# Performance work log

Measured on AMD Instinct MI355X. Metric: run time of the kernel, lower is better.

Reference implementation:

```python
import jax, jax.numpy as jnp
import numpy as np

B, N, EMB, HID, CODE, FEAT, L = 8, 96, 768, 384, 192, 768, 2
NEG = 1e30  # mask_logic constant


def _gru(x, h, Wih, Whh, bih, bhh):
    # torch.nn.GRUCell math; gate order r, z, n
    gi = x @ Wih.T + bih
    gh = h @ Whh.T + bhh
    ir, iz, inn = jnp.split(gi, 3, axis=-1)
    hr, hz, hn = jnp.split(gh, 3, axis=-1)
    r = jax.nn.sigmoid(ir + hr)
    z = jax.nn.sigmoid(iz + hz)
    n = jnp.tanh(inn + r * hn)
    return (1.0 - z) * n + z * h


def _node0(Hl, gc, gp):
    # node 0: C = gru_c(x, 0); P = gru_p(0, x); H1 = C + P
    x0 = Hl[:, 0]
    z0 = jnp.zeros_like(x0)
    h0 = _gru(x0, z0, *gc) + _gru(z0, x0, *gp)
    b, n, d = Hl.shape
    return jnp.zeros((b, n, d), Hl.dtype).at[:, 0].set(h0)


def _dag_scan(Hl, s_mask, aux, Wr0, Wr1, gc, gp, get_w):
    # sequential DAG recurrence: node i attends over nodes < i of the CURRENT layer's outputs
    b, n, d = Hl.shape
    buf0 = _node0(Hl, gc, gp)
    pos = jnp.arange(n)

    def step(buf, inp):
        i, q, s_row, aux_row = inp
        valid = pos < i                                  # growing history slice [:i]
        w = get_w(buf, q, aux_row, valid)                # (B,N), zero for j >= i
        s = s_row[:, :, None]
        V = (buf @ Wr0.T) * s + (buf @ Wr1.T) * (1.0 - s)  # speaker-relation values
        M = jnp.einsum('bn,bnd->bd', w, V)
        hn = _gru(q, M, *gc) + _gru(M, q, *gp)           # C + P
        return buf.at[:, i].set(hn), w

    xs = (jnp.arange(1, n),
          jnp.swapaxes(Hl[:, 1:], 0, 1),
          jnp.swapaxes(s_mask[:, 1:], 0, 1),
          jnp.swapaxes(aux[:, 1:], 0, 1))
    buf, ws = jax.lax.scan(step, buf0, xs)
    return buf, jnp.swapaxes(ws, 0, 1)  # H1 (B,N,D), attn rows 1..N-1 (B,N-1,N)


def _mlp(x, W0, b0, W1, b1):
    # out_mlp with mlp_layers=1 (dropout is identity in eval mode)
    return jax.nn.relu(x @ W0.T + b0) @ W1.T + b1


def _forward(features, adj, s_mask, s_mask_onehot,
             enc_fc1_W, enc_fc1_b, enc_gat_w, enc_gat_b, enc_Wr0, enc_Wr1,
             enc_gruc_Wih, enc_gruc_Whh, enc_gruc_bih, enc_gruc_bhh,
             enc_grup_Wih, enc_grup_Whh, enc_grup_bih, enc_grup_bhh,
             enc_mlp_W0, enc_mlp_b0, enc_mlp_W1, enc_mlp_b1,
             dec_fc1_W, dec_fc1_b, dec_Wr0, dec_Wr1,
             dec_gruc_Wih, dec_gruc_Whh, dec_gruc_bih, dec_gruc_bhh,
             dec_grup_Wih, dec_grup_Whh, dec_grup_bih, dec_grup_bhh,
             dec_mlp_W0, dec_mlp_b0, dec_mlp_W1, dec_mlp_b1,
             lengths):
    b, n, _ = features.shape
    I = jnp.broadcast_to(jnp.eye(n, dtype=features.dtype), (b, n, n))
    # ----- encoder -----
    Hs = [jax.nn.relu(features @ enc_fc1_W.T + enc_fc1_b)]
    adjB_list = [jnp.zeros((b, 1, n), features.dtype)]
    for l in range(L):
        gc = (enc_gruc_Wih[l], enc_gruc_Whh[l], enc_gruc_bih[l], enc_gruc_bhh[l])
        gp = (enc_grup_Wih[l], enc_grup_Whh[l], enc_grup_bih[l], enc_grup_bhh[l])
        wq, wk, gb = enc_gat_w[l, :HID], enc_gat_w[l, HID:], enc_gat_b[l]

        def get_w(buf, q, adj_row, valid, wq=wq, wk=wk, gb=gb):
            # GAT_encoder: alpha = Linear([q; K]) masked by adj over history (mask_logic)
            alpha = buf @ wk + (q @ wq)[:, None] + gb
            alpha = alpha - (1.0 - adj_row) * NEG
            alpha = jnp.where(valid[None, :], alpha, -jnp.inf)
            return jax.nn.softmax(alpha, axis=-1)

        H1, ws = _dag_scan(Hs[l], s_mask, adj, enc_Wr0[l], enc_Wr1[l], gc, gp, get_w)
        Hs.append(H1)
        # row 0 of adjB is zeros; rows 1..N-1 are zero-padded attention weights
        adjB_list.append(jnp.concatenate([jnp.zeros((b, 1, n), features.dtype), ws], axis=1))
    fU = _mlp(jnp.concatenate(Hs, axis=-1), enc_mlp_W0, enc_mlp_b0, enc_mlp_W1, enc_mlp_b1)
    # ----- decoder -----
    Hs = [jax.nn.relu(fU @ dec_fc1_W.T + dec_fc1_b)]
    for l in range(L):
        gc = (dec_gruc_Wih[l], dec_gruc_Whh[l], dec_gruc_bih[l], dec_gruc_bhh[l])
        gp = (dec_grup_Wih[l], dec_grup_Whh[l], dec_grup_bih[l], dec_grup_bhh[l])
        b_inv = jnp.linalg.solve(I, I - adjB_list[l + 1])

        def get_w(buf, q, w_row, valid):
            # GNN_decoder: uses b_inv[:, i, :i] directly as gather weights
            return jnp.where(valid[None, :], w_row, 0.0)

        H1, _ = _dag_scan(Hs[l], s_mask, b_inv, dec_Wr0[l], dec_Wr1[l], gc, gp, get_w)
        Hs.append(H1)
    logits = _mlp(jnp.concatenate(Hs, axis=-1), dec_mlp_W0, dec_mlp_b0, dec_mlp_W1, dec_mlp_b1)
    feature_map = jnp.linalg.solve(I, I - adjB_list[2])
    return logits, feature_map


def setup_inputs() -> dict:
    key = jax.random.key(0)
    ks = iter(jax.random.split(key, 48))

    def rn(*shape):
        return jax.random.normal(next(ks), shape, jnp.float32) * 0.05

    return dict(
        features=jax.random.normal(next(ks), (B, N, EMB), jnp.float32),
        adj=jax.random.randint(next(ks), (B, N, N), 0, 2).astype(jnp.float32),
        s_mask=jax.random.randint(next(ks), (B, N, N), 0, 2).astype(jnp.float32),
        s_mask_onehot=jnp.zeros((B, N, N, 2), jnp.float32),
        lengths=jax.random.randint(next(ks), (B,), 1, N),
        enc_fc1_W=rn(HID, EMB), enc_fc1_b=rn(HID),
        enc_gat_w=rn(L, 2 * HID), enc_gat_b=rn(L),
        enc_Wr0=rn(L, HID, HID), enc_Wr1=rn(L, HID, HID),
        enc_gruc_Wih=rn(L, 3 * HID, HID), enc_gruc_Whh=rn(L, 3 * HID, HID),
        enc_gruc_bih=rn(L, 3 * HID), enc_gruc_bhh=rn(L, 3 * HID),
        enc_grup_Wih=rn(L, 3 * HID, HID), enc_grup_Whh=rn(L, 3 * HID, HID),
        enc_grup_bih=rn(L, 3 * HID), enc_grup_bhh=rn(L, 3 * HID),
        enc_mlp_W0=rn(HID, (L + 1) * HID), enc_mlp_b0=rn(HID),
        enc_mlp_W1=rn(CODE, HID), enc_mlp_b1=rn(CODE),
        dec_fc1_W=rn(HID, CODE), dec_fc1_b=rn(HID),
        dec_Wr0=rn(L, HID, HID), dec_Wr1=rn(L, HID, HID),
        dec_gruc_Wih=rn(L, 3 * HID, HID), dec_gruc_Whh=rn(L, 3 * HID, HID),
        dec_gruc_bih=rn(L, 3 * HID), dec_gruc_bhh=rn(L, 3 * HID),
        dec_grup_Wih=rn(L, 3 * HID, HID), dec_grup_Whh=rn(L, 3 * HID, HID),
        dec_grup_bih=rn(L, 3 * HID), dec_grup_bhh=rn(L, 3 * HID),
        dec_mlp_W0=rn(HID, (L + 1) * HID), dec_mlp_b0=rn(HID),
        dec_mlp_W1=rn(FEAT, HID), dec_mlp_b1=rn(FEAT),
    )


def reference(features, adj, s_mask, s_mask_onehot, lengths,
              enc_fc1_W, enc_fc1_b, enc_gat_w, enc_gat_b, enc_Wr0, enc_Wr1,
              enc_gruc_Wih, enc_gruc_Whh, enc_gruc_bih, enc_gruc_bhh,
              enc_grup_Wih, enc_grup_Whh, enc_grup_bih, enc_grup_bhh,
              enc_mlp_W0, enc_mlp_b0, enc_mlp_W1, enc_mlp_b1,
              dec_fc1_W, dec_fc1_b, dec_Wr0, dec_Wr1,
              dec_gruc_Wih, dec_gruc_Whh, dec_gruc_bih, dec_gruc_bhh,
              dec_grup_Wih, dec_grup_Whh, dec_grup_bih, dec_grup_bhh,
              dec_mlp_W0, dec_mlp_b0, dec_mlp_W1, dec_mlp_b1):
    return _forward(features, adj, s_mask, s_mask_onehot,
                    enc_fc1_W, enc_fc1_b, enc_gat_w, enc_gat_b, enc_Wr0, enc_Wr1,
                    enc_gruc_Wih, enc_gruc_Whh, enc_gruc_bih, enc_gruc_bhh,
                    enc_grup_Wih, enc_grup_Whh, enc_grup_bih, enc_grup_bhh,
                    enc_mlp_W0, enc_mlp_b0, enc_mlp_W1, enc_mlp_b1,
                    dec_fc1_W, dec_fc1_b, dec_Wr0, dec_Wr1,
                    dec_gruc_Wih, dec_gruc_Whh, dec_gruc_bih, dec_gruc_bhh,
                    dec_grup_Wih, dec_grup_Whh, dec_grup_bih, dec_grup_bhh,
                    dec_mlp_W0, dec_mlp_b0, dec_mlp_W1, dec_mlp_b1,
                    lengths)
```

## Files before the change

kernel.cpp:

```cpp
#include <hip/hip_runtime.h>
#include <math.h>

#define B_    8
#define N_    96
#define EMB_  768
#define HID_  384
#define GID_  1152
#define CONC_ 1152
#define CODE_ 192
#define FEAT_ 768
#define NSL_  64
#define SD_   6
#define NRW_  42

__device__ __forceinline__ float sigf(float x) { return 1.0f / (1.0f + expf(-x)); }

__device__ __forceinline__ void atstf(float* p, float v) {
  __hip_atomic_store(p, v, __ATOMIC_RELAXED, __HIP_MEMORY_SCOPE_AGENT);
}
__device__ __forceinline__ float atldf(const float* p) {
  return __hip_atomic_load((float*)p, __ATOMIC_RELAXED, __HIP_MEMORY_SCOPE_AGENT);
}
__device__ __forceinline__ float dot4(float4 a, float4 b) {
  return fmaf(a.x, b.x, fmaf(a.y, b.y, fmaf(a.z, b.z, a.w * b.w)));
}

template<int RELU>
__global__ __launch_bounds__(256)
void gemm_bias(const float* __restrict__ A, int lda,
               const float* __restrict__ W,
               const float* __restrict__ bias,
               float* __restrict__ C, int ldc, int K)
{
  __shared__ float As[16][68];
  __shared__ float Bs[16][68];
  const int tid = threadIdx.x;
  const int m0 = blockIdx.y * 64;
  const int n0 = blockIdx.x * 64;
  const int lr = tid >> 2;
  const int lc = (tid & 3) * 4;
  const int ty = tid >> 4, tx = tid & 15;
  float acc[4][4] = {};
  for (int k0 = 0; k0 < K; k0 += 16) {
    float4 a4 = *(const float4*)(A + (size_t)(m0 + lr) * lda + k0 + lc);
    float4 b4 = *(const float4*)(W + (size_t)(n0 + lr) * K + k0 + lc);
    As[lc+0][lr] = a4.x; As[lc+1][lr] = a4.y; As[lc+2][lr] = a4.z; As[lc+3][lr] = a4.w;
    Bs[lc+0][lr] = b4.x; Bs[lc+1][lr] = b4.y; Bs[lc+2][lr] = b4.z; Bs[lc+3][lr] = b4.w;
    __syncthreads();
#pragma unroll
    for (int k = 0; k < 16; ++k) {
      float av[4], bv[4];
#pragma unroll
      for (int i = 0; i < 4; ++i) av[i] = As[k][ty*4+i];
#pragma unroll
      for (int j = 0; j < 4; ++j) bv[j] = Bs[k][tx*4+j];
#pragma unroll
      for (int i = 0; i < 4; ++i)
#pragma unroll
        for (int j = 0; j < 4; ++j) acc[i][j] = fmaf(av[i], bv[j], acc[i][j]);
    }
    __syncthreads();
  }
#pragma unroll
  for (int i = 0; i < 4; ++i) {
    int m = m0 + ty*4 + i;
#pragma unroll
    for (int j = 0; j < 4; ++j) {
      int n = n0 + tx*4 + j;
      float v = acc[i][j] + bias[n];
      if (RELU) v = fmaxf(v, 0.0f);
      C[(size_t)m * ldc + n] = v;
    }
  }
}

__global__ __launch_bounds__(256)
void gemm_bias2(const float* __restrict__ A,
                const float* __restrict__ W0, const float* __restrict__ b0,
                float* __restrict__ C0,
                const float* __restrict__ W1, const float* __restrict__ b1,
                float* __restrict__ C1)
{
  const float* W    = (blockIdx.z == 0) ? W0 : W1;
  const float* bias = (blockIdx.z == 0) ? b0 : b1;
  float*       C    = (blockIdx.z == 0) ? C0 : C1;
  __shared__ float As[16][68];
  __shared__ float Bs[16][68];
  const int tid = threadIdx.x;
  const int m0 = blockIdx.y * 64;
  const int n0 = blockIdx.x * 64;
  const int lr = tid >> 2;
  const int lc = (tid & 3) * 4;
  const int ty = tid >> 4, tx = tid & 15;
  float acc[4][4] = {};
  for (int k0 = 0; k0 < HID_; k0 += 16) {
    float4 a4 = *(const float4*)(A + (size_t)(m0 + lr) * CONC_ + k0 + lc);
    float4 b4 = *(const float4*)(W + (size_t)(n0 + lr) * HID_ + k0 + lc);
    As[lc+0][lr] = a4.x; As[lc+1][lr] = a4.y; As[lc+2][lr] = a4.z; As[lc+3][lr] = a4.w;
    Bs[lc+0][lr] = b4.x; Bs[lc+1][lr] = b4.y; Bs[lc+2][lr] = b4.z; Bs[lc+3][lr] = b4.w;
    __syncthreads();
#pragma unroll
    for (int k = 0; k < 16; ++k) {
      float av[4], bv[4];
#pragma unroll
      for (int i = 0; i < 4; ++i) av[i] = As[k][ty*4+i];
#pragma unroll
      for (int j = 0; j < 4; ++j) bv[j] = Bs[k][tx*4+j];
#pragma unroll
      for (int i = 0; i < 4; ++i)
#pragma unroll
        for (int j = 0; j < 4; ++j) acc[i][j] = fmaf(av[i], bv[j], acc[i][j]);
    }
    __syncthreads();
  }
#pragma unroll
  for (int i = 0; i < 4; ++i) {
    int m = m0 + ty*4 + i;
#pragma unroll
    for (int j = 0; j < 4; ++j) {
      int n = n0 + tx*4 + j;
      C[(size_t)m * GID_ + n] = acc[i][j] + bias[n];
    }
  }
}

__global__ __launch_bounds__(256)
void prod_kernel(const float* __restrict__ Ac, const float* __restrict__ Ap,
                 const float* __restrict__ W0, const float* __restrict__ W1,
                 float* __restrict__ G)
{
  const float* A = (blockIdx.z < 2) ? Ac : Ap;
  const float* W = (blockIdx.z & 1) ? W1 : W0;
  float* C = G + (size_t)blockIdx.z * GID_ * HID_;
  __shared__ float As[16][68];
  __shared__ float Bs[16][68];
  const int tid = threadIdx.x;
  const int m0 = blockIdx.y * 64;
  const int n0 = blockIdx.x * 64;
  const int lr = tid >> 2;
  const int lc = (tid & 3) * 4;
  const int lr2 = tid & 63, kq = tid >> 6;
  const int ty = tid >> 4, tx = tid & 15;
  float acc[4][4] = {};
  for (int k0 = 0; k0 < HID_; k0 += 16) {
    float4 a4 = *(const float4*)(A + (size_t)(m0 + lr) * HID_ + k0 + lc);
    As[lc+0][lr] = a4.x; As[lc+1][lr] = a4.y; As[lc+2][lr] = a4.z; As[lc+3][lr] = a4.w;
#pragma unroll
    for (int u = 0; u < 4; ++u) {
      int kl = kq * 4 + u;
      Bs[kl][lr2] = W[(size_t)(k0 + kl) * HID_ + n0 + lr2];
    }
    __syncthreads();
#pragma unroll
    for (int k = 0; k < 16; ++k) {
      float av[4], bv[4];
#pragma unroll
      for (int i = 0; i < 4; ++i) av[i] = As[k][ty*4+i];
#pragma unroll
      for (int j = 0; j < 4; ++j) bv[j] = Bs[k][tx*4+j];
#pragma unroll
      for (int i = 0; i < 4; ++i)
#pragma unroll
        for (int j = 0; j < 4; ++j) acc[i][j] = fmaf(av[i], bv[j], acc[i][j]);
    }
    __syncthreads();
  }
#pragma unroll
  for (int i = 0; i < 4; ++i)
#pragma unroll
    for (int j = 0; j < 4; ++j)
      C[(size_t)(m0 + ty*4 + i) * HID_ + n0 + tx*4 + j] = acc[i][j];
}

struct ScanP {
  const float* Hl;
  float*       bufC;
  float*       hnX;
  const float* G;
  const float* GIc;
  const float* GHp;
  const float* bhhc;
  const float* bihp;
  const float* Wr0;
  const float* Wr1;
  const float* wk;
  const float* mask;
  const float* smask;
  float*       adjB;
};

template<int ENC>
__global__ __launch_bounds__(256, 2)
void scan_kernel(ScanP p)
{
  const int tid  = threadIdx.x;
  const int b    = blockIdx.x >> 6;
  const int sl   = blockIdx.x & 63;
  const int j0   = sl * SD_;
  const int team = tid >> 4, lane = tid & 15;

  __shared__ __align__(16) float stage[HID_];
  __shared__ float ws0[N_], ws1[N_], s_sm[N_];
  __shared__ float alpha[N_];
  __shared__ float dots[48];
  __shared__ float red4a[4], red4b[4];
  __shared__ float sh_aknew;
  __shared__ float PA[NRW_ * 97];
  __shared__ float PB[NRW_ * 97];

  for (int k = tid; k < NRW_ * 97; k += 256) { PA[k] = 0.f; PB[k] = 0.f; }

  float4 wAr[3][6], wBr[3][6];
#pragma unroll
  for (int u = 0; u < 3; ++u) {
    const int r = team + 16 * u;
    const float *Aptr, *Bptr;
    if (r < 36) {
      const int g = r / 6, jl = r % 6;
      const size_t off = (size_t)((g % 3) * HID_ + j0 + jl) * HID_;
      const float* base = p.G + (g < 3 ? 0 : 2) * (size_t)GID_ * HID_;
      Aptr = base + off;
      Bptr = base + (size_t)GID_ * HID_ + off;
    } else if (r < 42) {
      const int jl = r - 36;
      Aptr = p.Wr0 + (size_t)(j0 + jl) * HID_;
      Bptr = p.Wr1 + (size_t)(j0 + jl) * HID_;
    } else if (r == 42 && ENC) {
      Aptr = p.wk; Bptr = p.wk;
    } else {
      Aptr = p.Wr0; Bptr = p.Wr1;
    }
#pragma unroll
    for (int m = 0; m < 6; ++m) {
      wAr[u][m] = ((const float4*)Aptr)[lane + 16*m];
      wBr[u][m] = ((const float4*)Bptr)[lane + 16*m];
    }
  }
  float bh0=0, bh1=0, bh2=0, bi0=0, bi1=0, bi2=0;
  if (tid < SD_) {
    int j = j0 + tid;
    bh0 = p.bhhc[j]; bh1 = p.bhhc[HID_ + j]; bh2 = p.bhhc[2*HID_ + j];
    bi0 = p.bihp[j]; bi1 = p.bihp[HID_ + j]; bi2 = p.bihp[2*HID_ + j];
  }

#define BULK_STAGE(SRC)                                                      \
  do {                                                                       \
    if (tid < NSL_) {                                                        \
      const float* f_ = (SRC) + tid * SD_;                                   \
      while (__float_as_uint(atldf(f_)) == 0xFFFFFFFFu) {}                   \
    }                                                                        \
    __syncthreads();                                                         \
    {                                                                        \
      float v0 = atldf((SRC) + tid);                                         \
      while (__float_as_uint(v0) == 0xFFFFFFFFu) v0 = atldf((SRC) + tid);    \
      stage[tid] = v0;                                                       \
      if (tid < HID_ - 256) {                                                \
        float v1 = atldf((SRC) + 256 + tid);                                 \
        while (__float_as_uint(v1) == 0xFFFFFFFFu)                           \
          v1 = atldf((SRC) + 256 + tid);                                     \
        stage[256 + tid] = v1;                                               \
      }                                                                      \
    }                                                                        \
    __syncthreads();                                                         \
  } while (0)

  if (tid < SD_) {
    int j = j0 + tid;
    const float* gi = p.GIc + (size_t)(b * N_) * GID_;
    const float* gh = p.GHp + (size_t)(b * N_) * GID_;
    float rc = sigf(gi[j] + bh0);
    float zc = sigf(gi[HID_ + j] + bh1);
    float nc = tanhf(gi[2*HID_ + j] + rc * bh2);
    float outc = (1.0f - zc) * nc;
    float rp = sigf(bi0 + gh[j]);
    float zp = sigf(bi1 + gh[HID_ + j]);
    float np = tanhf(bi2 + rp * gh[2*HID_ + j]);
    float x0 = p.Hl[(size_t)(b * N_) * CONC_ + j];
    float h0 = outc + (1.0f - zp) * np + zp * x0;
    p.bufC[(size_t)(b * N_) * CONC_ + j] = h0;
    atstf(&p.hnX[(size_t)(b * N_) * HID_ + j], h0);
  }
  __syncthreads();

  for (int i = 1; i < N_; ++i) {
    float pf_gi0=0, pf_gi1=0, pf_gi2=0, pf_gh0=0, pf_gh1=0, pf_gh2=0, pf_q=0;
    if (tid < SD_) {
      int j = j0 + tid;
      const float* gi = p.GIc + ((size_t)b * N_ + i) * GID_;
      const float* gh = p.GHp + ((size_t)b * N_ + i) * GID_;
      pf_gi0 = gi[j]; pf_gi1 = gi[HID_ + j]; pf_gi2 = gi[2*HID_ + j];
      pf_gh0 = gh[j]; pf_gh1 = gh[HID_ + j]; pf_gh2 = gh[2*HID_ + j];
      pf_q   = p.Hl[((size_t)b * N_ + i) * CONC_ + j];
    }
    float pf_mrow = 0.0f;
    if (tid < N_) {
      pf_mrow = p.mask[((size_t)b * N_ + i) * N_ + tid];
      s_sm[tid] = p.smask[((size_t)b * N_ + i) * N_ + tid];
    }

    const float* srcH = p.hnX + (size_t)(b * N_ + (i - 1)) * HID_;
    BULK_STAGE(srcH);
    const float4* st4 = (const float4*)stage;
    float4 hreg[6];
#pragma unroll
    for (int m = 0; m < 6; ++m) hreg[m] = st4[lane + 16*m];

#pragma unroll
    for (int u = 0; u < 3; ++u) {
      const int r = team + 16 * u;
      float a = 0.f, bv = 0.f;
#pragma unroll
      for (int m = 0; m < 6; ++m) {
        a  += dot4(wAr[u][m], hreg[m]);
        bv += dot4(wBr[u][m], hreg[m]);
      }
#pragma unroll
      for (int mm = 8; mm; mm >>= 1) {
        a  += __shfl_xor(a, mm);
        bv += __shfl_xor(bv, mm);
      }
      if (lane == 0) {
        if (r < NRW_) { PA[r * 97 + (i - 1)] = a; PB[r * 97 + (i - 1)] = bv; }
        else if (ENC && r == 42) sh_aknew = a;
      }
    }
    __syncthreads();

    if (ENC) {
      if (tid == 0) alpha[i - 1] = sh_aknew;
      float av = -3.0e38f;
      if (tid < i) {
        float ak = (tid == i - 1) ? sh_aknew : alpha[tid];
        av = ak - (1.0f - pf_mrow) * 1e30f;
      }
      float v = av;
#pragma unroll
      for (int m = 32; m; m >>= 1) v = fmaxf(v, __shfl_xor(v, m));
      if ((tid & 63) == 0) red4a[tid >> 6] = v;
      __syncthreads();
      float mx = fmaxf(fmaxf(red4a[0], red4a[1]), fmaxf(red4a[2], red4a[3]));
      float e = (tid < i) ? expf(av - mx) : 0.0f;
      v = e;
#pragma unroll
      for (int m = 32; m; m >>= 1) v += __shfl_xor(v, m);
      if ((tid & 63) == 0) red4b[tid >> 6] = v;
      __syncthreads();
      float ssum = red4b[0] + red4b[1] + red4b[2] + red4b[3];
      if (tid < N_) {
        float w = (tid < i) ? e / ssum : 0.0f;
        float sv = s_sm[tid];
        ws0[tid] = w * sv;
        ws1[tid] = w - w * sv;
        if (sl == 0) p.adjB[((size_t)b * N_ + i) * N_ + tid] = w;
      }
      __syncthreads();
    } else {
      if (tid < N_) {
        float w = (tid < i) ? -pf_mrow : 0.0f;
        float sv = s_sm[tid];
        ws0[tid] = w * sv;
        ws1[tid] = w - w * sv;
      }
      __syncthreads();
    }

    {
      float wsr0[6], wsr1[6];
#pragma unroll
      for (int k = 0; k < 6; ++k) {
        wsr0[k] = ws0[lane + 16*k];
        wsr1[k] = ws1[lane + 16*k];
      }
#pragma unroll
      for (int u = 0; u < 3; ++u) {
        const int r = team + 16 * u;
        if (r < NRW_) {
          float acc = 0.f;
#pragma unroll
          for (int k = 0; k < 6; ++k) {
            int n = lane + 16*k;
            acc = fmaf(wsr0[k], PA[r * 97 + n], fmaf(wsr1[k], PB[r * 97 + n], acc));
          }
#pragma unroll
          for (int mm = 8; mm; mm >>= 1) acc += __shfl_xor(acc, mm);
          if (lane == 0) dots[r] = acc;
        }
      }
    }
    __syncthreads();

    if (tid < SD_) {
      int j = j0 + tid;
      float Mj = dots[36 + tid];
      float rc = sigf(pf_gi0 + dots[tid] + bh0);
      float zc = sigf(pf_gi1 + dots[6 + tid] + bh1);
      float nc = tanhf(pf_gi2 + rc * (dots[12 + tid] + bh2));
      float outc = (1.0f - zc) * nc + zc * Mj;
      float rp = sigf(dots[18 + tid] + bi0 + pf_gh0);
      float zp = sigf(dots[24 + tid] + bi1 + pf_gh1);
      float np = tanhf(dots[30 + tid] + bi2 + rp * pf_gh2);
      float hv = outc + (1.0f - zp) * np + zp * pf_q;
      p.bufC[((size_t)b * N_ + i) * CONC_ + j] = hv;
      atstf(&p.hnX[((size_t)b * N_ + i) * HID_ + j], hv);
    }
    __syncthreads();
  }
#undef BULK_STAGE
}

__global__ __launch_bounds__(256)
void fmap_kernel(const float* __restrict__ adjB2, float* __restrict__ out)
{
  int idx = blockIdx.x * 256 + threadIdx.x;
  if (idx < B_ * N_ * N_) {
    int j = idx % N_;
    int i = (idx / N_) % N_;
    float a = (i == 0) ? 0.0f : adjB2[idx];
    out[idx] = ((i == j) ? 1.0f : 0.0f) - a;
  }
}

extern "C" void kernel_launch(void* const* d_in, const int* in_sizes, int n_in,
                              void* d_out, int out_size, void* d_ws, size_t ws_size,
                              hipStream_t stream)
{
  (void)in_sizes; (void)n_in; (void)out_size; (void)ws_size;
  const float* features     = (const float*)d_in[0];
  const float* adj          = (const float*)d_in[1];
  const float* s_mask       = (const float*)d_in[2];
  const float* enc_fc1_W    = (const float*)d_in[5];
  const float* enc_fc1_b    = (const float*)d_in[6];
  const float* enc_gat_w    = (const float*)d_in[7];
  const float* enc_Wr0      = (const float*)d_in[9];
  const float* enc_Wr1      = (const float*)d_in[10];
  const float* enc_gruc_Wih = (const float*)d_in[11];
  const float* enc_gruc_Whh = (const float*)d_in[12];
  const float* enc_gruc_bih = (const float*)d_in[13];
  const float* enc_gruc_bhh = (const float*)d_in[14];
  const float* enc_grup_Wih = (const float*)d_in[15];
  const float* enc_grup_Whh = (const float*)d_in[16];
  const float* enc_grup_bih = (const float*)d_in[17];
  const float* enc_grup_bhh = (const float*)d_in[18];
  const float* enc_mlp_W0   = (const float*)d_in[19];
  const float* enc_mlp_b0   = (const float*)d_in[20];
  const float* enc_mlp_W1   = (const float*)d_in[21];
  const float* enc_mlp_b1   = (const float*)d_in[22];
  const float* dec_fc1_W    = (const float*)d_in[23];
  const float* dec_fc1_b    = (const float*)d_in[24];
  const float* dec_Wr0      = (const float*)d_in[25];
  const float* dec_Wr1      = (const float*)d_in[26];
  const float* dec_gruc_Wih = (const float*)d_in[27];
  const float* dec_gruc_Whh = (const float*)d_in[28];
  const float* dec_gruc_bih = (const float*)d_in[29];
  const float* dec_gruc_bhh = (const float*)d_in[30];
  const float* dec_grup_Wih = (const float*)d_in[31];
  const float* dec_grup_Whh = (const float*)d_in[32];
  const float* dec_grup_bih = (const float*)d_in[33];
  const float* dec_grup_bhh = (const float*)d_in[34];
  const float* dec_mlp_W0   = (const float*)d_in[35];
  const float* dec_mlp_b0   = (const float*)d_in[36];
  const float* dec_mlp_W1   = (const float*)d_in[37];
  const float* dec_mlp_b1   = (const float*)d_in[38];

  float* ws = (float*)d_ws;
  size_t o = 0;
  float* Hse   = ws + o; o += (size_t)B_ * N_ * CONC_;
  float* Hsd   = ws + o; o += (size_t)B_ * N_ * CONC_;
  float* GIc   = ws + o; o += (size_t)B_ * N_ * GID_;
  float* GHp   = ws + o; o += (size_t)B_ * N_ * GID_;
  float* adjB1 = ws + o; o += (size_t)B_ * N_ * N_;
  float* adjB2 = ws + o; o += (size_t)B_ * N_ * N_;
  float* fU    = ws + o; o += (size_t)B_ * N_ * CODE_;
  float* Tmp   = ws + o; o += (size_t)B_ * N_ * HID_;
  float* hnX4  = ws + o; o += (size_t)4 * B_ * N_ * HID_;
  float* Gbuf  = ws + o; o += (size_t)4 * GID_ * HID_;
  const size_t hn_elems = (size_t)B_ * N_ * HID_;

  const dim3 blk(256);
  float* logits = (float*)d_out;
  float* fmap   = (float*)d_out + (size_t)B_ * N_ * FEAT_;

  hipMemsetAsync(hnX4, 0xFF, 4 * hn_elems * sizeof(float), stream);

  gemm_bias<1><<<dim3(6, 12), blk, 0, stream>>>(features, EMB_, enc_fc1_W, enc_fc1_b,
                                                Hse, CONC_, EMB_);
  for (int l = 0; l < 2; ++l) {
    const float* Hl = Hse + l * HID_;
    gemm_bias2<<<dim3(18, 12, 2), blk, 0, stream>>>(Hl,
        enc_gruc_Wih + (size_t)l * GID_ * HID_, enc_gruc_bih + l * GID_, GIc,
        enc_grup_Whh + (size_t)l * GID_ * HID_, enc_grup_bhh + l * GID_, GHp);
    prod_kernel<<<dim3(6, 18, 4), blk, 0, stream>>>(
        enc_gruc_Whh + (size_t)l * GID_ * HID_, enc_grup_Wih + (size_t)l * GID_ * HID_,
        enc_Wr0 + (size_t)l * HID_ * HID_, enc_Wr1 + (size_t)l * HID_ * HID_, Gbuf);
    ScanP p;
    p.Hl = Hl; p.bufC = Hse + (l + 1) * HID_;
    p.hnX = hnX4 + (size_t)l * hn_elems; p.G = Gbuf;
    p.GIc = GIc; p.GHp = GHp;
    p.bhhc = enc_gruc_bhh + l * GID_;
    p.bihp = enc_grup_bih + l * GID_;
    p.Wr0 = enc_Wr0 + (size_t)l * HID_ * HID_;
    p.Wr1 = enc_Wr1 + (size_t)l * HID_ * HID_;
    p.wk = enc_gat_w + l * 2 * HID_ + HID_;
    p.mask = adj; p.smask = s_mask;
    p.adjB = (l == 0) ? adjB1 : adjB2;
    scan_kernel<1><<<dim3(512), blk, 0, stream>>>(p);
  }
  gemm_bias<1><<<dim3(6, 12), blk, 0, stream>>>(Hse, CONC_, enc_mlp_W0, enc_mlp_b0,
                                                Tmp, HID_, CONC_);
  gemm_bias<0><<<dim3(3, 12), blk, 0, stream>>>(Tmp, HID_, enc_mlp_W1, enc_mlp_b1,
                                                fU, CODE_, HID_);
  gemm_bias<1><<<dim3(6, 12), blk, 0, stream>>>(fU, CODE_, dec_fc1_W, dec_fc1_b,
                                                Hsd, CONC_, CODE_);
  for (int l = 0; l < 2; ++l) {
    const float* Hl = Hsd + l * HID_;
    gemm_bias2<<<dim3(18, 12, 2), blk, 0, stream>>>(Hl,
        dec_gruc_Wih + (size_t)l * GID_ * HID_, dec_gruc_bih + l * GID_, GIc,
        dec_grup_Whh + (size_t)l * GID_ * HID_, dec_grup_bhh + l * GID_, GHp);
    prod_kernel<<<dim3(6, 18, 4), blk, 0, stream>>>(
        dec_gruc_Whh + (size_t)l * GID_ * HID_, dec_grup_Wih + (size_t)l * GID_ * HID_,
        dec_Wr0 + (size_t)l * HID_ * HID_, dec_Wr1 + (size_t)l * HID_ * HID_, Gbuf);
    ScanP p;
    p.Hl = Hl; p.bufC = Hsd + (l + 1) * HID_;
    p.hnX = hnX4 + (size_t)(2 + l) * hn_elems; p.G = Gbuf;
    p.GIc = GIc; p.GHp = GHp;
    p.bhhc = dec_gruc_bhh + l * GID_;
    p.bihp = dec_grup_bih + l * GID_;
    p.Wr0 = dec_Wr0 + (size_t)l * HID_ * HID_;
    p.Wr1 = dec_Wr1 + (size_t)l * HID_ * HID_;
    p.wk = nullptr;
    p.mask = (l == 0) ? adjB1 : adjB2;
    p.smask = s_mask;
    p.adjB = nullptr;
    scan_kernel<0><<<dim3(512), blk, 0, stream>>>(p);
  }
  gemm_bias<1><<<dim3(6, 12), blk, 0, stream>>>(Hsd, CONC_, dec_mlp_W0, dec_mlp_b0,
                                                Tmp, HID_, CONC_);
  gemm_bias<0><<<dim3(12, 12), blk, 0, stream>>>(Tmp, HID_, dec_mlp_W1, dec_mlp_b1,
                                                 logits, FEAT_, HID_);
  fmap_kernel<<<dim3((B_ * N_ * N_ + 255) / 256), blk, 0, stream>>>(adjB2, fmap);
}
```

Baseline: 1.900 ms.

## Fuse both DAG layers into one wavefront-pipelined scan kernel

Merges the two per-layer sequential scan kernels into a single kernel that computes layer-1 node t-1 in the same iteration as layer-0 node t. Layer-1 input projections are computed inline from the staged layer-0 output instead of by a separate GEMM. The shared history buffers are stored as bf16 so two layers' worth fit in LDS. This removes a kernel launch and a full serial pass per encoder/decoder. The cost is that weights are now read from global memory every step rather than held in registers, and bf16 history reduces precision.

```diff
diff --git a/kernel.cpp b/kernel.cpp
--- a/kernel.cpp
+++ b/kernel.cpp
@@ -12,6 +12,7 @@
 #define NSL_  64
 #define SD_   6
 #define NRW_  42
+#define HP_   98
 
 __device__ __forceinline__ float sigf(float x) { return 1.0f / (1.0f + expf(-x)); }
 
@@ -23,6 +24,14 @@
 }
 __device__ __forceinline__ float dot4(float4 a, float4 b) {
   return fmaf(a.x, b.x, fmaf(a.y, b.y, fmaf(a.z, b.z, a.w * b.w)));
+}
+__device__ __forceinline__ unsigned short f2bf(float f) {
+  unsigned u = __float_as_uint(f);
+  u += 0x7fffu + ((u >> 16) & 1u);
+  return (unsigned short)(u >> 16);
+}
+__device__ __forceinline__ float bfu(unsigned short s) {
+  return __uint_as_float(((unsigned)s) << 16);
 }
 
 template<int RELU>
@@ -172,26 +181,115 @@
       C[(size_t)(m0 + ty*4 + i) * HID_ + n0 + tx*4 + j] = acc[i][j];
 }
 
-struct ScanP {
-  const float* Hl;
-  float*       bufC;
-  float*       hnX;
-  const float* G;
-  const float* GIc;
-  const float* GHp;
-  const float* bhhc;
-  const float* bihp;
-  const float* Wr0;
-  const float* Wr1;
-  const float* wk;
-  const float* mask;
-  const float* smask;
-  float*       adjB;
+struct Scan2P {
+  const float* Hl0; float* bufC0; float* bufC1;
+  float* hnX0; float* hnX1;
+  const float* G0; const float* G1;
+  const float* GIc; const float* GHp;
+  const float* bhhc0; const float* bihp0;
+  const float* Wr00; const float* Wr10; const float* wk0;
+  const float* Wr01; const float* Wr11; const float* wk1;
+  const float* Wihc1; const float* bihc1;
+  const float* Whhp1; const float* bhhp1;
+  const float* bhhc1; const float* bihp1;
+  const float* mask0; const float* mask1; const float* smask;
+  float* adjB0; float* adjB1o;
 };
+
+__device__ __forceinline__ void bulk_stage(const float* src, float* stg, int tid)
+{
+  if (tid < NSL_) {
+    const float* f_ = src + tid * SD_;
+    while (__float_as_uint(atldf(f_)) == 0xFFFFFFFFu) {}
+  }
+  __syncthreads();
+  {
+    float v0 = atldf(src + tid);
+    while (__float_as_uint(v0) == 0xFFFFFFFFu) v0 = atldf(src + tid);
+    stg[tid] = v0;
+    if (tid < HID_ - 256) {
+      float v1 = atldf(src + 256 + tid);
+      while (__float_as_uint(v1) == 0xFFFFFFFFu) v1 = atldf(src + 256 + tid);
+      stg[256 + tid] = v1;
+    }
+  }
+  __syncthreads();
+}
+
+template<int ENC>
+__device__ __forceinline__ void make_w(
+    int i, int tid, float pf_m, float* alpha, const float* s_sm,
+    float* ws0, float* ws1, float* red4a, float* red4b,
+    const float* shak, float* adjRow)
+{
+  if (ENC) {
+    float ak_new = *shak;
+    if (tid == 0) alpha[i - 1] = ak_new;
+    float av = -3.0e38f;
+    if (tid < i) {
+      float ak = (tid == i - 1) ? ak_new : alpha[tid];
+      av = ak - (1.0f - pf_m) * 1e30f;
+    }
+    float v = av;
+#pragma unroll
+    for (int m = 32; m; m >>= 1) v = fmaxf(v, __shfl_xor(v, m));
+    if ((tid & 63) == 0) red4a[tid >> 6] = v;
+    __syncthreads();
+    float mx = fmaxf(fmaxf(red4a[0], red4a[1]), fmaxf(red4a[2], red4a[3]));
+    float e = (tid < i) ? expf(av - mx) : 0.0f;
+    v = e;
+#pragma unroll
+    for (int m = 32; m; m >>= 1) v += __shfl_xor(v, m);
+    if ((tid & 63) == 0) red4b[tid >> 6] = v;
+    __syncthreads();
+    float ssum = red4b[0] + red4b[1] + red4b[2] + red4b[3];
+    if (tid < N_) {
+      float w = (tid < i) ? e / ssum : 0.0f;
+      float sv = s_sm[tid];
+      ws0[tid] = w * sv;
+      ws1[tid] = w - w * sv;
+      if (adjRow) adjRow[tid] = w;
+    }
+    __syncthreads();
+  } else {
+    if (tid < N_) {
+      float w = (tid < i) ? -pf_m : 0.0f;
+      float sv = s_sm[tid];
+      ws0[tid] = w * sv;
+      ws1[tid] = w - w * sv;
+    }
+    __syncthreads();
+  }
+}
+
+__device__ __forceinline__ void hist_dots(
+    const unsigned short* PA, const unsigned short* PB,
+    const float* ws0, const float* ws1, float* dots, int team, int lane)
+{
+  float wsr0[6], wsr1[6];
+#pragma unroll
+  for (int k = 0; k < 6; ++k) { wsr0[k] = ws0[lane + 16*k]; wsr1[k] = ws1[lane + 16*k]; }
+#pragma unroll
+  for (int u = 0; u < 3; ++u) {
+    const int r = team + 16 * u;
+    if (r < NRW_) {
+      float acc = 0.f;
+#pragma unroll
+      for (int k = 0; k < 6; ++k) {
+        int n = lane + 16*k;
+        acc = fmaf(wsr0[k], bfu(PA[r * HP_ + n]),
+              fmaf(wsr1[k], bfu(PB[r * HP_ + n]), acc));
+      }
+#pragma unroll
+      for (int mm = 8; mm; mm >>= 1) acc += __shfl_xor(acc, mm);
+      if (lane == 0) dots[r] = acc;
+    }
+  }
+}
 
 template<int ENC>
 __global__ __launch_bounds__(256, 2)
-void scan_kernel(ScanP p)
+void scan2_kernel(Scan2P p)
 {
   const int tid  = threadIdx.x;
   const int b    = blockIdx.x >> 6;
@@ -199,213 +297,232 @@
   const int j0   = sl * SD_;
   const int team = tid >> 4, lane = tid & 15;
 
-  __shared__ __align__(16) float stage[HID_];
+  __shared__ __align__(16) float stage0[HID_];
+  __shared__ __align__(16) float stage1[HID_];
+  __shared__ unsigned short PA0[NRW_*HP_], PB0[NRW_*HP_];
+  __shared__ unsigned short PA1[NRW_*HP_], PB1[NRW_*HP_];
   __shared__ float ws0[N_], ws1[N_], s_sm[N_];
-  __shared__ float alpha[N_];
+  __shared__ float alpha0[N_], alpha1[N_];
   __shared__ float dots[48];
+  __shared__ float gdI[18], gdH[18];
   __shared__ float red4a[4], red4b[4];
-  __shared__ float sh_aknew;
-  __shared__ float PA[NRW_ * 97];
-  __shared__ float PB[NRW_ * 97];
-
-  for (int k = tid; k < NRW_ * 97; k += 256) { PA[k] = 0.f; PB[k] = 0.f; }
-
-  float4 wAr[3][6], wBr[3][6];
+  __shared__ float sh_ak;
+
+  for (int k = tid; k < NRW_*HP_; k += 256) { PA0[k]=0; PB0[k]=0; PA1[k]=0; PB1[k]=0; }
+
+  const float4 *pA0[3], *pB0[3], *pA1[3], *pB1[3];
 #pragma unroll
   for (int u = 0; u < 3; ++u) {
     const int r = team + 16 * u;
-    const float *Aptr, *Bptr;
+    const float *A0,*B0,*A1,*B1;
     if (r < 36) {
       const int g = r / 6, jl = r % 6;
       const size_t off = (size_t)((g % 3) * HID_ + j0 + jl) * HID_;
-      const float* base = p.G + (g < 3 ? 0 : 2) * (size_t)GID_ * HID_;
-      Aptr = base + off;
-      Bptr = base + (size_t)GID_ * HID_ + off;
+      const float* b0 = p.G0 + (g < 3 ? 0 : 2) * (size_t)GID_ * HID_;
+      const float* b1 = p.G1 + (g < 3 ? 0 : 2) * (size_t)GID_ * HID_;
+      A0 = b0 + off; B0 = b0 + (size_t)GID_ * HID_ + off;
+      A1 = b1 + off; B1 = b1 + (size_t)GID_ * HID_ + off;
     } else if (r < 42) {
       const int jl = r - 36;
-      Aptr = p.Wr0 + (size_t)(j0 + jl) * HID_;
-      Bptr = p.Wr1 + (size_t)(j0 + jl) * HID_;
+      A0 = p.Wr00 + (size_t)(j0 + jl) * HID_; B0 = p.Wr10 + (size_t)(j0 + jl) * HID_;
+      A1 = p.Wr01 + (size_t)(j0 + jl) * HID_; B1 = p.Wr11 + (size_t)(j0 + jl) * HID_;
     } else if (r == 42 && ENC) {
-      Aptr = p.wk; Bptr = p.wk;
+      A0 = p.wk0; B0 = p.wk0; A1 = p.wk1; B1 = p.wk1;
     } else {
-      Aptr = p.Wr0; Bptr = p.Wr1;
-    }
-#pragma unroll
-    for (int m = 0; m < 6; ++m) {
-      wAr[u][m] = ((const float4*)Aptr)[lane + 16*m];
-      wBr[u][m] = ((const float4*)Bptr)[lane + 16*m];
-    }
-  }
-  float bh0=0, bh1=0, bh2=0, bi0=0, bi1=0, bi2=0;
+      A0 = p.Wr00; B0 = p.Wr10; A1 = p.Wr01; B1 = p.Wr11;
+    }
+    pA0[u]=(const float4*)A0; pB0[u]=(const float4*)B0;
+    pA1[u]=(const float4*)A1; pB1[u]=(const float4*)B1;
+  }
+  const float4 *pGI[2], *pGH[2]; float bGI[2], bGH[2];
+#pragma unroll
+  for (int u = 0; u < 2; ++u) {
+    const int r2 = team + 16 * u;
+    if (r2 < 18) {
+      const int g = r2 / 6, jl = r2 % 6;
+      const size_t row = (size_t)(g * HID_ + j0 + jl);
+      pGI[u] = (const float4*)(p.Wihc1 + row * HID_);
+      pGH[u] = (const float4*)(p.Whhp1 + row * HID_);
+      bGI[u] = p.bihc1[row]; bGH[u] = p.bhhp1[row];
+    } else {
+      pGI[u] = (const float4*)p.Wihc1; pGH[u] = (const float4*)p.Whhp1;
+      bGI[u] = 0.f; bGH[u] = 0.f;
+    }
+  }
+  float c0h0=0,c0h1=0,c0h2=0,c0i0=0,c0i1=0,c0i2=0;
+  float c1h0=0,c1h1=0,c1h2=0,c1i0=0,c1i1=0,c1i2=0;
   if (tid < SD_) {
     int j = j0 + tid;
-    bh0 = p.bhhc[j]; bh1 = p.bhhc[HID_ + j]; bh2 = p.bhhc[2*HID_ + j];
-    bi0 = p.bihp[j]; bi1 = p.bihp[HID_ + j]; bi2 = p.bihp[2*HID_ + j];
-  }
-
-#define BULK_STAGE(SRC)                                                      \
-  do {                                                                       \
-    if (tid < NSL_) {                                                        \
-      const float* f_ = (SRC) + tid * SD_;                                   \
-      while (__float_as_uint(atldf(f_)) == 0xFFFFFFFFu) {}                   \
-    }                                                                        \
-    __syncthreads();                                                         \
-    {                                                                        \
-      float v0 = atldf((SRC) + tid);                                         \
-      while (__float_as_uint(v0) == 0xFFFFFFFFu) v0 = atldf((SRC) + tid);    \
-      stage[tid] = v0;                                                       \
-      if (tid < HID_ - 256) {                                                \
-        float v1 = atldf((SRC) + 256 + tid);                                 \
-        while (__float_as_uint(v1) == 0xFFFFFFFFu)                           \
-          v1 = atldf((SRC) + 256 + tid);                                     \
-        stage[256 + tid] = v1;                                               \
-      }                                                                      \
-    }                                                                        \
-    __syncthreads();                                                         \
-  } while (0)
+    c0h0=p.bhhc0[j]; c0h1=p.bhhc0[HID_+j]; c0h2=p.bhhc0[2*HID_+j];
+    c0i0=p.bihp0[j]; c0i1=p.bihp0[HID_+j]; c0i2=p.bihp0[2*HID_+j];
+    c1h0=p.bhhc1[j]; c1h1=p.bhhc1[HID_+j]; c1h2=p.bhhc1[2*HID_+j];
+    c1i0=p.bihp1[j]; c1i1=p.bihp1[HID_+j]; c1i2=p.bihp1[2*HID_+j];
+  }
 
   if (tid < SD_) {
     int j = j0 + tid;
     const float* gi = p.GIc + (size_t)(b * N_) * GID_;
     const float* gh = p.GHp + (size_t)(b * N_) * GID_;
-    float rc = sigf(gi[j] + bh0);
-    float zc = sigf(gi[HID_ + j] + bh1);
-    float nc = tanhf(gi[2*HID_ + j] + rc * bh2);
+    float rc = sigf(gi[j] + c0h0);
+    float zc = sigf(gi[HID_ + j] + c0h1);
+    float nc = tanhf(gi[2*HID_ + j] + rc * c0h2);
     float outc = (1.0f - zc) * nc;
-    float rp = sigf(bi0 + gh[j]);
-    float zp = sigf(bi1 + gh[HID_ + j]);
-    float np = tanhf(bi2 + rp * gh[2*HID_ + j]);
-    float x0 = p.Hl[(size_t)(b * N_) * CONC_ + j];
+    float rp = sigf(c0i0 + gh[j]);
+    float zp = sigf(c0i1 + gh[HID_ + j]);
+    float np = tanhf(c0i2 + rp * gh[2*HID_ + j]);
+    float x0 = p.Hl0[(size_t)(b * N_) * CONC_ + j];
     float h0 = outc + (1.0f - zp) * np + zp * x0;
-    p.bufC[(size_t)(b * N_) * CONC_ + j] = h0;
-    atstf(&p.hnX[(size_t)(b * N_) * HID_ + j], h0);
+    p.bufC0[(size_t)(b * N_) * CONC_ + j] = h0;
+    atstf(&p.hnX0[(size_t)(b * N_) * HID_ + j], h0);
   }
   __syncthreads();
 
-  for (int i = 1; i < N_; ++i) {
-    float pf_gi0=0, pf_gi1=0, pf_gi2=0, pf_gh0=0, pf_gh1=0, pf_gh2=0, pf_q=0;
-    if (tid < SD_) {
-      int j = j0 + tid;
-      const float* gi = p.GIc + ((size_t)b * N_ + i) * GID_;
-      const float* gh = p.GHp + ((size_t)b * N_ + i) * GID_;
-      pf_gi0 = gi[j]; pf_gi1 = gi[HID_ + j]; pf_gi2 = gi[2*HID_ + j];
-      pf_gh0 = gh[j]; pf_gh1 = gh[HID_ + j]; pf_gh2 = gh[2*HID_ + j];
-      pf_q   = p.Hl[((size_t)b * N_ + i) * CONC_ + j];
-    }
-    float pf_mrow = 0.0f;
-    if (tid < N_) {
-      pf_mrow = p.mask[((size_t)b * N_ + i) * N_ + tid];
-      s_sm[tid] = p.smask[((size_t)b * N_ + i) * N_ + tid];
-    }
-
-    const float* srcH = p.hnX + (size_t)(b * N_ + (i - 1)) * HID_;
-    BULK_STAGE(srcH);
-    const float4* st4 = (const float4*)stage;
-    float4 hreg[6];
-#pragma unroll
-    for (int m = 0; m < 6; ++m) hreg[m] = st4[lane + 16*m];
-
-#pragma unroll
-    for (int u = 0; u < 3; ++u) {
-      const int r = team + 16 * u;
-      float a = 0.f, bv = 0.f;
-#pragma unroll
-      for (int m = 0; m < 6; ++m) {
-        a  += dot4(wAr[u][m], hreg[m]);
-        bv += dot4(wBr[u][m], hreg[m]);
-      }
-#pragma unroll
-      for (int mm = 8; mm; mm >>= 1) {
-        a  += __shfl_xor(a, mm);
-        bv += __shfl_xor(bv, mm);
-      }
-      if (lane == 0) {
-        if (r < NRW_) { PA[r * 97 + (i - 1)] = a; PB[r * 97 + (i - 1)] = bv; }
-        else if (ENC && r == 42) sh_aknew = a;
-      }
-    }
-    __syncthreads();
-
-    if (ENC) {
-      if (tid == 0) alpha[i - 1] = sh_aknew;
-      float av = -3.0e38f;
-      if (tid < i) {
-        float ak = (tid == i - 1) ? sh_aknew : alpha[tid];
-        av = ak - (1.0f - pf_mrow) * 1e30f;
-      }
-      float v = av;
-#pragma unroll
-      for (int m = 32; m; m >>= 1) v = fmaxf(v, __shfl_xor(v, m));
-      if ((tid & 63) == 0) red4a[tid >> 6] = v;
+  for (int t = 1; t <= N_; ++t) {
+    const bool doA = (t < N_);
+    float a_gi0=0,a_gi1=0,a_gi2=0,a_gh0=0,a_gh1=0,a_gh2=0,a_q=0,a_m=0;
+    if (doA) {
+      if (tid < SD_) {
+        int j = j0 + tid;
+        const float* gi = p.GIc + ((size_t)b * N_ + t) * GID_;
+        const float* gh = p.GHp + ((size_t)b * N_ + t) * GID_;
+        a_gi0 = gi[j]; a_gi1 = gi[HID_ + j]; a_gi2 = gi[2*HID_ + j];
+        a_gh0 = gh[j]; a_gh1 = gh[HID_ + j]; a_gh2 = gh[2*HID_ + j];
+        a_q   = p.Hl0[((size_t)b * N_ + t) * CONC_ + j];
+      }
+      if (tid < N_) {
+        a_m = p.mask0[((size_t)b * N_ + t) * N_ + tid];
+        s_sm[tid] = p.smask[((size_t)b * N_ + t) * N_ + tid];
+      }
+    }
+    bulk_stage(p.hnX0 + (size_t)(b * N_ + t - 1) * HID_, stage0, tid);
+    if (doA) {
+      const float4* st = (const float4*)stage0;
+      float4 hr[6];
+#pragma unroll
+      for (int m = 0; m < 6; ++m) hr[m] = st[lane + 16*m];
+#pragma unroll
+      for (int u = 0; u < 3; ++u) {
+        const int r = team + 16 * u;
+        float a = 0.f, bv = 0.f;
+#pragma unroll
+        for (int m = 0; m < 6; ++m) {
+          a  += dot4(pA0[u][lane + 16*m], hr[m]);
+          bv += dot4(pB0[u][lane + 16*m], hr[m]);
+        }
+#pragma unroll
+        for (int mm = 8; mm; mm >>= 1) { a += __shfl_xor(a, mm); bv += __shfl_xor(bv, mm); }
+        if (lane == 0) {
+          if (r < NRW_) { PA0[r*HP_ + (t-1)] = f2bf(a); PB0[r*HP_ + (t-1)] = f2bf(bv); }
+          else if (ENC && r == 42) sh_ak = a;
+        }
+      }
       __syncthreads();
-      float mx = fmaxf(fmaxf(red4a[0], red4a[1]), fmaxf(red4a[2], red4a[3]));
-      float e = (tid < i) ? expf(av - mx) : 0.0f;
-      v = e;
-#pragma unroll
-      for (int m = 32; m; m >>= 1) v += __shfl_xor(v, m);
-      if ((tid & 63) == 0) red4b[tid >> 6] = v;
+      float* adjRow = (ENC && sl == 0) ? (p.adjB0 + ((size_t)b * N_ + t) * N_) : nullptr;
+      make_w<ENC>(t, tid, a_m, alpha0, s_sm, ws0, ws1, red4a, red4b, &sh_ak, adjRow);
+      hist_dots(PA0, PB0, ws0, ws1, dots, team, lane);
       __syncthreads();
-      float ssum = red4b[0] + red4b[1] + red4b[2] + red4b[3];
-      if (tid < N_) {
-        float w = (tid < i) ? e / ssum : 0.0f;
-        float sv = s_sm[tid];
-        ws0[tid] = w * sv;
-        ws1[tid] = w - w * sv;
-        if (sl == 0) p.adjB[((size_t)b * N_ + i) * N_ + tid] = w;
+      if (tid < SD_) {
+        int j = j0 + tid;
+        float Mj = dots[36 + tid];
+        float rc = sigf(a_gi0 + dots[tid] + c0h0);
+        float zc = sigf(a_gi1 + dots[6 + tid] + c0h1);
+        float nc = tanhf(a_gi2 + rc * (dots[12 + tid] + c0h2));
+        float outc = (1.0f - zc) * nc + zc * Mj;
+        float rp = sigf(dots[18 + tid] + c0i0 + a_gh0);
+        float zp = sigf(dots[24 + tid] + c0i1 + a_gh1);
+        float np = tanhf(dots[30 + tid] + c0i2 + rp * a_gh2);
+        float hv = outc + (1.0f - zp) * np + zp * a_q;
+        p.bufC0[((size_t)b * N_ + t) * CONC_ + j] = hv;
+        atstf(&p.hnX0[((size_t)b * N_ + t) * HID_ + j], hv);
+      }
+    }
+    {
+      const float4* st = (const float4*)stage0;
+      float4 hr[6];
+#pragma unroll
+      for (int m = 0; m < 6; ++m) hr[m] = st[lane + 16*m];
+#pragma unroll
+      for (int u = 0; u < 2; ++u) {
+        const int r2 = team + 16 * u;
+        float a = 0.f, bv = 0.f;
+#pragma unroll
+        for (int m = 0; m < 6; ++m) {
+          a  += dot4(pGI[u][lane + 16*m], hr[m]);
+          bv += dot4(pGH[u][lane + 16*m], hr[m]);
+        }
+#pragma unroll
+        for (int mm = 8; mm; mm >>= 1) { a += __shfl_xor(a, mm); bv += __shfl_xor(bv, mm); }
+        if (lane == 0 && r2 < 18) { gdI[r2] = a + bGI[u]; gdH[r2] = bv + bGH[u]; }
+      }
+    }
+    if (t == 1) {
+      __syncthreads();
+      if (tid < SD_) {
+        int j = j0 + tid;
+        float rc = sigf(gdI[tid] + c1h0);
+        float zc = sigf(gdI[6 + tid] + c1h1);
+        float nc = tanhf(gdI[12 + tid] + rc * c1h2);
+        float outc = (1.0f - zc) * nc;
+        float rp = sigf(c1i0 + gdH[tid]);
+        float zp = sigf(c1i1 + gdH[6 + tid]);
+        float np = tanhf(c1i2 + rp * gdH[12 + tid]);
+        float x0 = stage0[j];
+        float hv = outc + (1.0f - zp) * np + zp * x0;
+        p.bufC1[(size_t)(b * N_) * CONC_ + j] = hv;
+        atstf(&p.hnX1[(size_t)(b * N_) * HID_ + j], hv);
       }
       __syncthreads();
     } else {
+      const int i1 = t - 1;
+      float b_m = 0.f;
       if (tid < N_) {
-        float w = (tid < i) ? -pf_mrow : 0.0f;
-        float sv = s_sm[tid];
-        ws0[tid] = w * sv;
-        ws1[tid] = w - w * sv;
-      }
-      __syncthreads();
-    }
-
-    {
-      float wsr0[6], wsr1[6];
-#pragma unroll
-      for (int k = 0; k < 6; ++k) {
-        wsr0[k] = ws0[lane + 16*k];
-        wsr1[k] = ws1[lane + 16*k];
-      }
+        b_m = p.mask1[((size_t)b * N_ + i1) * N_ + tid];
+        s_sm[tid] = p.smask[((size_t)b * N_ + i1) * N_ + tid];
+      }
+      bulk_stage(p.hnX1 + (size_t)(b * N_ + t - 2) * HID_, stage1, tid);
+      const float4* st1 = (const float4*)stage1;
+      float4 hr[6];
+#pragma unroll
+      for (int m = 0; m < 6; ++m) hr[m] = st1[lane + 16*m];
 #pragma unroll
       for (int u = 0; u < 3; ++u) {
         const int r = team + 16 * u;
-        if (r < NRW_) {
-          float acc = 0.f;
-#pragma unroll
-          for (int k = 0; k < 6; ++k) {
-            int n = lane + 16*k;
-            acc = fmaf(wsr0[k], PA[r * 97 + n], fmaf(wsr1[k], PB[r * 97 + n], acc));
-          }
-#pragma unroll
-          for (int mm = 8; mm; mm >>= 1) acc += __shfl_xor(acc, mm);
-          if (lane == 0) dots[r] = acc;
+        float a = 0.f, bv = 0.f;
+#pragma unroll
+        for (int m = 0; m < 6; ++m) {
+          a  += dot4(pA1[u][lane + 16*m], hr[m]);
+          bv += dot4(pB1[u][lane + 16*m], hr[m]);
         }
-      }
-    }
-    __syncthreads();
-
-    if (tid < SD_) {
-      int j = j0 + tid;
-      float Mj = dots[36 + tid];
-      float rc = sigf(pf_gi0 + dots[tid] + bh0);
-      float zc = sigf(pf_gi1 + dots[6 + tid] + bh1);
-      float nc = tanhf(pf_gi2 + rc * (dots[12 + tid] + bh2));
-      float outc = (1.0f - zc) * nc + zc * Mj;
-      float rp = sigf(dots[18 + tid] + bi0 + pf_gh0);
-      float zp = sigf(dots[24 + tid] + bi1 + pf_gh1);
-      float np = tanhf(dots[30 + tid] + bi2 + rp * pf_gh2);
-      float hv = outc + (1.0f - zp) * np + zp * pf_q;
-      p.bufC[((size_t)b * N_ + i) * CONC_ + j] = hv;
-      atstf(&p.hnX[((size_t)b * N_ + i) * HID_ + j], hv);
-    }
-    __syncthreads();
-  }
-#undef BULK_STAGE
+#pragma unroll
+        for (int mm = 8; mm; mm >>= 1) { a += __shfl_xor(a, mm); bv += __shfl_xor(bv, mm); }
+        if (lane == 0) {
+          if (r < NRW_) { PA1[r*HP_ + (t-2)] = f2bf(a); PB1[r*HP_ + (t-2)] = f2bf(bv); }
+          else if (ENC && r == 42) sh_ak = a;
+        }
+      }
+      __syncthreads();
+      float* adjRow1 = (ENC && sl == 0) ? (p.adjB1o + ((size_t)b * N_ + i1) * N_) : nullptr;
+      make_w<ENC>(i1, tid, b_m, alpha1, s_sm, ws0, ws1, red4a, red4b, &sh_ak, adjRow1);
+      hist_dots(PA1, PB1, ws0, ws1, dots, team, lane);
+      __syncthreads();
+      if (tid < SD_) {
+        int j = j0 + tid;
+        float Mj = dots[36 + tid];
+        float rc = sigf(gdI[tid] + dots[tid] + c1h0);
+        float zc = sigf(gdI[6 + tid] + dots[6 + tid] + c1h1);
+        float nc = tanhf(gdI[12 + tid] + rc * (dots[12 + tid] + c1h2));
+        float outc = (1.0f - zc) * nc + zc * Mj;
+        float rp = sigf(dots[18 + tid] + c1i0 + gdH[tid]);
+        float zp = sigf(dots[24 + tid] + c1i1 + gdH[6 + tid]);
+        float np = tanhf(dots[30 + tid] + c1i2 + rp * gdH[12 + tid]);
+        float q1 = stage0[j];
+        float hv = outc + (1.0f - zp) * np + zp * q1;
+        p.bufC1[((size_t)b * N_ + i1) * CONC_ + j] = hv;
+        atstf(&p.hnX1[((size_t)b * N_ + i1) * HID_ + j], hv);
+      }
+      __syncthreads();
+    }
+  }
 }
 
 __global__ __launch_bounds__(256)
@@ -473,8 +590,9 @@
   float* fU    = ws + o; o += (size_t)B_ * N_ * CODE_;
   float* Tmp   = ws + o; o += (size_t)B_ * N_ * HID_;
   float* hnX4  = ws + o; o += (size_t)4 * B_ * N_ * HID_;
-  float* Gbuf  = ws + o; o += (size_t)4 * GID_ * HID_;
+  float* Gbuf  = ws + o; o += (size_t)8 * GID_ * HID_;
   const size_t hn_elems = (size_t)B_ * N_ * HID_;
+  const size_t Gly = (size_t)4 * GID_ * HID_;
 
   const dim3 blk(256);
   float* logits = (float*)d_out;
@@ -484,26 +602,29 @@
 
   gemm_bias<1><<<dim3(6, 12), blk, 0, stream>>>(features, EMB_, enc_fc1_W, enc_fc1_b,
                                                 Hse, CONC_, EMB_);
-  for (int l = 0; l < 2; ++l) {
-    const float* Hl = Hse + l * HID_;
-    gemm_bias2<<<dim3(18, 12, 2), blk, 0, stream>>>(Hl,
-        enc_gruc_Wih + (size_t)l * GID_ * HID_, enc_gruc_bih + l * GID_, GIc,
-        enc_grup_Whh + (size_t)l * GID_ * HID_, enc_grup_bhh + l * GID_, GHp);
-    prod_kernel<<<dim3(6, 18, 4), blk, 0, stream>>>(
-        enc_gruc_Whh + (size_t)l * GID_ * HID_, enc_grup_Wih + (size_t)l * GID_ * HID_,
-        enc_Wr0 + (size_t)l * HID_ * HID_, enc_Wr1 + (size_t)l * HID_ * HID_, Gbuf);
-    ScanP p;
-    p.Hl = Hl; p.bufC = Hse + (l + 1) * HID_;
-    p.hnX = hnX4 + (size_t)l * hn_elems; p.G = Gbuf;
+  gemm_bias2<<<dim3(18, 12, 2), blk, 0, stream>>>(Hse,
+      enc_gruc_Wih, enc_gruc_bih, GIc, enc_grup_Whh, enc_grup_bhh, GHp);
+  prod_kernel<<<dim3(6, 18, 4), blk, 0, stream>>>(
+      enc_gruc_Whh, enc_grup_Wih, enc_Wr0, enc_Wr1, Gbuf);
+  prod_kernel<<<dim3(6, 18, 4), blk, 0, stream>>>(
+      enc_gruc_Whh + (size_t)GID_ * HID_, enc_grup_Wih + (size_t)GID_ * HID_,
+      enc_Wr0 + (size_t)HID_ * HID_, enc_Wr1 + (size_t)HID_ * HID_, Gbuf + Gly);
+  {
+    Scan2P p;
+    p.Hl0 = Hse; p.bufC0 = Hse + HID_; p.bufC1 = Hse + 2 * HID_;
+    p.hnX0 = hnX4; p.hnX1 = hnX4 + hn_elems;
+    p.G0 = Gbuf; p.G1 = Gbuf + Gly;
     p.GIc = GIc; p.GHp = GHp;
-    p.bhhc = enc_gruc_bhh + l * GID_;
-    p.bihp = enc_grup_bih + l * GID_;
-    p.Wr0 = enc_Wr0 + (size_t)l * HID_ * HID_;
-    p.Wr1 = enc_Wr1 + (size_t)l * HID_ * HID_;
-    p.wk = enc_gat_w + l * 2 * HID_ + HID_;
-    p.mask = adj; p.smask = s_mask;
-    p.adjB = (l == 0) ? adjB1 : adjB2;
-    scan_kernel<1><<<dim3(512), blk, 0, stream>>>(p);
+    p.bhhc0 = enc_gruc_bhh; p.bihp0 = enc_grup_bih;
+    p.Wr00 = enc_Wr0; p.Wr10 = enc_Wr1; p.wk0 = enc_gat_w + HID_;
+    p.Wr01 = enc_Wr0 + (size_t)HID_ * HID_; p.Wr11 = enc_Wr1 + (size_t)HID_ * HID_;
+    p.wk1 = enc_gat_w + 3 * HID_;
+    p.Wihc1 = enc_gruc_Wih + (size_t)GID_ * HID_; p.bihc1 = enc_gruc_bih + GID_;
+    p.Whhp1 = enc_grup_Whh + (size_t)GID_ * HID_; p.bhhp1 = enc_grup_bhh + GID_;
+    p.bhhc1 = enc_gruc_bhh + GID_; p.bihp1 = enc_grup_bih + GID_;
+    p.mask0 = adj; p.mask1 = adj; p.smask = s_mask;
+    p.adjB0 = adjB1; p.adjB1o = adjB2;
+    scan2_kernel<1><<<dim3(512), blk, 0, stream>>>(p);
   }
   gemm_bias<1><<<dim3(6, 12), blk, 0, stream>>>(Hse, CONC_, enc_mlp_W0, enc_mlp_b0,
                                                 Tmp, HID_, CONC_);
@@ -511,27 +632,29 @@
                                                 fU, CODE_, HID_);
   gemm_bias<1><<<dim3(6, 12), blk, 0, stream>>>(fU, CODE_, dec_fc1_W, dec_fc1_b,
                                                 Hsd, CONC_, CODE_);
-  for (int l = 0; l < 2; ++l) {
-    const float* Hl = Hsd + l * HID_;
-    gemm_bias2<<<dim3(18, 12, 2), blk, 0, stream>>>(Hl,
-        dec_gruc_Wih + (size_t)l * GID_ * HID_, dec_gruc_bih + l * GID_, GIc,
-        dec_grup_Whh + (size_t)l * GID_ * HID_, dec_grup_bhh + l * GID_, GHp);
-    prod_kernel<<<dim3(6, 18, 4), blk, 0, stream>>>(
-        dec_gruc_Whh + (size_t)l * GID_ * HID_, dec_grup_Wih + (size_t)l * GID_ * HID_,
-        dec_Wr0 + (size_t)l * HID_ * HID_, dec_Wr1 + (size_t)l * HID_ * HID_, Gbuf);
-    ScanP p;
-    p.Hl = Hl; p.bufC = Hsd + (l + 1) * HID_;
-    p.hnX = hnX4 + (size_t)(2 + l) * hn_elems; p.G = Gbuf;
+  gemm_bias2<<<dim3(18, 12, 2), blk, 0, stream>>>(Hsd,
+      dec_gruc_Wih, dec_gruc_bih, GIc, dec_grup_Whh, dec_grup_bhh, GHp);
+  prod_kernel<<<dim3(6, 18, 4), blk, 0, stream>>>(
+      dec_gruc_Whh, dec_grup_Wih, dec_Wr0, dec_Wr1, Gbuf);
+  prod_kernel<<<dim3(6, 18, 4), blk, 0, stream>>>(
+      dec_gruc_Whh + (size_t)GID_ * HID_, dec_grup_Wih + (size_t)GID_ * HID_,
+      dec_Wr0 + (size_t)HID_ * HID_, dec_Wr1 + (size_t)HID_ * HID_, Gbuf + Gly);
+  {
+    Scan2P p;
+    p.Hl0 = Hsd; p.bufC0 = Hsd + HID_; p.bufC1 = Hsd + 2 * HID_;
+    p.hnX0 = hnX4 + 2 * hn_elems; p.hnX1 = hnX4 + 3 * hn_elems;
+    p.G0 = Gbuf; p.G1 = Gbuf + Gly;
     p.GIc = GIc; p.GHp = GHp;
-    p.bhhc = dec_gruc_bhh + l * GID_;
-    p.bihp = dec_grup_bih + l * GID_;
-    p.Wr0 = dec_Wr0 + (size_t)l * HID_ * HID_;
-    p.Wr1 = dec_Wr1 + (size_t)l * HID_ * HID_;
-    p.wk = nullptr;
-    p.mask = (l == 0) ? adjB1 : adjB2;
-    p.smask = s_mask;
-    p.adjB = nullptr;
-    scan_kernel<0><<<dim3(512), blk, 0, stream>>>(p);
+    p.bhhc0 = dec_gruc_bhh; p.bihp0 = dec_grup_bih;
+    p.Wr00 = dec_Wr0; p.Wr10 = dec_Wr1; p.wk0 = nullptr;
+    p.Wr01 = dec_Wr0 + (size_t)HID_ * HID_; p.Wr11 = dec_Wr1 + (size_t)HID_ * HID_;
+    p.wk1 = nullptr;
+    p.Wihc1 = dec_gruc_Wih + (size_t)GID_ * HID_; p.bihc1 = dec_gruc_bih + GID_;
+    p.Whhp1 = dec_grup_Whh + (size_t)GID_ * HID_; p.bhhp1 = dec_grup_bhh + GID_;
+    p.bhhc1 = dec_gruc_bhh + GID_; p.bihp1 = dec_grup_bih + GID_;
+    p.mask0 = adjB1; p.mask1 = adjB2; p.smask = s_mask;
+    p.adjB0 = nullptr; p.adjB1o = nullptr;
+    scan2_kernel<0><<<dim3(512), blk, 0, stream>>>(p);
   }
   gemm_bias<1><<<dim3(6, 12), blk, 0, stream>>>(Hsd, CONC_, dec_mlp_W0, dec_mlp_b0,
                                                 Tmp, HID_, CONC_);
```

After: 4.692 ms. 2.47x slower.
